# Kernel optimization log

Hardware: AMD Instinct MI355X
Metric: run time of the kernel (lower is better)

## Reference

```python
import jax, jax.numpy as jnp
import numpy as np

B, N, DIM = 2, 4096, 512
HEADS, DIM_HEAD = 8, 64
INNER = HEADS * DIM_HEAD  # 512
SCALE = DIM_HEAD ** -0.5
LN_EPS = 1e-5


def setup_inputs() -> dict:
    key = jax.random.key(0)
    ks = jax.random.split(key, 4)
    x = jax.random.normal(ks[0], (B, N, DIM), dtype=jnp.float32)
    # weights stored as [in, out] for plain matmul
    w_qkv = jax.random.normal(ks[1], (DIM, 3 * INNER), dtype=jnp.float32) * (DIM ** -0.5)
    ln_gamma = jnp.ones((INNER,), dtype=jnp.float32)
    ln_beta = jnp.zeros((INNER,), dtype=jnp.float32)
    w_out = jax.random.normal(ks[2], (INNER, DIM), dtype=jnp.float32) * (INNER ** -0.5)
    b_out = jnp.zeros((DIM,), dtype=jnp.float32)
    return {"x": x, "w_qkv": w_qkv, "ln_gamma": ln_gamma, "ln_beta": ln_beta,
            "w_out": w_out, "b_out": b_out}


def _layernorm(x, gamma, beta):
    mu = jnp.mean(x, axis=-1, keepdims=True)
    var = jnp.mean(jnp.square(x - mu), axis=-1, keepdims=True)
    return (x - mu) * jax.lax.rsqrt(var + LN_EPS) * gamma + beta


def reference(x, w_qkv, ln_gamma, ln_beta, w_out, b_out):
    b, n, _ = x.shape
    qkv = x @ w_qkv                                   # [b, n, 3*inner]
    q, k, v = jnp.split(qkv, 3, axis=-1)
    def to_heads(t):
        return t.reshape(b, n, HEADS, DIM_HEAD).transpose(0, 2, 1, 3)  # [b,h,n,d]
    q, k, v = to_heads(q), to_heads(k), to_heads(v)
    dots = jnp.einsum('bhid,bhjd->bhij', q, k) * SCALE  # [b,h,n,n]
    attn = jax.nn.relu(dots)                            # non-softmax rectified attention
    out = jnp.einsum('bhij,bhjd->bhid', attn, v)        # [b,h,n,d]
    out = out.transpose(0, 2, 1, 3).reshape(b, n, INNER)
    out = _layernorm(out, ln_gamma, ln_beta)
    return out @ w_out + b_out                          # [b,n,dim]
```

## Files before the change

### kernel.cpp

```cpp
#include <hip/hip_runtime.h>
#include <stdint.h>
#include <stddef.h>

typedef __bf16 bf16;
typedef bf16 bf16x4 __attribute__((ext_vector_type(4)));
typedef bf16 bf16x8 __attribute__((ext_vector_type(8)));
typedef float f32x4 __attribute__((ext_vector_type(4)));

#define DEVI static __device__ __forceinline__


DEVI f32x4 mfma16(bf16x8 a, bf16x8 b, f32x4 c) {
  return __builtin_amdgcn_mfma_f32_16x16x32_bf16(a, b, c, 0, 0, 0);
}

DEVI void gload_lds16(const bf16* g, bf16* lds) {
  __builtin_amdgcn_global_load_lds(
      (const __attribute__((address_space(1))) unsigned int*)g,
      (__attribute__((address_space(3))) unsigned int*)lds, 16, 0, 0);
}

DEVI int sigma64(int r) { return (r & 0x23) | ((r & 0xC) << 1) | ((r & 0x10) >> 2); }


__global__ __launch_bounds__(256) void cvt_kernel(const float* __restrict__ in,
                                                  bf16* __restrict__ out, int n4) {
  int i = blockIdx.x * blockDim.x + threadIdx.x;
  const int stride = gridDim.x * blockDim.x;
  for (; i < n4; i += stride) {
    f32x4 v = reinterpret_cast<const f32x4*>(in)[i];
    bf16x4 o;
    o[0] = (bf16)v[0]; o[1] = (bf16)v[1]; o[2] = (bf16)v[2]; o[3] = (bf16)v[3];
    reinterpret_cast<bf16x4*>(out)[i] = o;
  }
}

__global__ __launch_bounds__(256) void tcvt_kernel(const float* __restrict__ in,
                                                   bf16* __restrict__ out, int Kd, int Nd) {
  __shared__ bf16 T[64 * 80];
  const int k0 = blockIdx.y * 64, n0 = blockIdx.x * 64;
  const int r = threadIdx.x >> 2;
  const int c0 = (threadIdx.x & 3) * 16;
  const float* src = in + (size_t)(k0 + r) * Nd + n0 + c0;
#pragma unroll
  for (int j = 0; j < 16; ++j) T[(c0 + j) * 80 + r] = (bf16)src[j];
  __syncthreads();
  bf16* dst = out + (size_t)(n0 + r) * Kd + k0 + c0;
  const bf16* s = T + r * 80 + c0;
#pragma unroll
  for (int j = 0; j < 2; ++j)
    *reinterpret_cast<bf16x8*>(dst + j * 8) =
        *reinterpret_cast<const bf16x8*>(s + j * 8);
}

template <int EPI>
__global__ __launch_bounds__(256) void gemm_kernel(
    const bf16* __restrict__ A, const bf16* __restrict__ BT,
    bf16* __restrict__ qo, bf16* __restrict__ ko, bf16* __restrict__ vto,
    const float* __restrict__ bias, float* __restrict__ fo) {
  constexpr int K = 512;
  __shared__ __align__(16) bf16 SM[4 * 128 * 64];
  const int lane = threadIdx.x & 63;
  const int w = threadIdx.x >> 6;
  const int hi = lane >> 4;
  const int wm = w >> 1, wn = w & 1;
  const int m0 = blockIdx.y * 128, n0 = blockIdx.x * 128;
  const int sl = lane >> 3;
  const int ssc = ((lane & 7) ^ sl) * 8;

  auto AsB = [&](int bi) { return SM + bi * 8192; };
  auto BsB = [&](int bi) { return SM + 16384 + bi * 8192; };

  auto stage = [&](int bi, int kt) {
    const int k0 = kt * 64;
#pragma unroll
    for (int c = 0; c < 4; ++c) {
      const int ca = w * 4 + c;
      const int trow = ca * 8 + sl;
      gload_lds16(A + (size_t)(m0 + trow) * K + k0 + ssc, AsB(bi) + ca * 512);
      gload_lds16(BT + (size_t)(n0 + trow) * K + k0 + ssc, BsB(bi) + ca * 512);
    }
  };

  f32x4 acc[4][4];
#pragma unroll
  for (int i = 0; i < 4; ++i)
#pragma unroll
    for (int j = 0; j < 4; ++j) acc[i][j] = {0.f, 0.f, 0.f, 0.f};

  stage(0, 0);
  asm volatile("s_waitcnt vmcnt(0)" ::: "memory");
  __builtin_amdgcn_s_barrier();

  for (int kt = 0; kt < K / 64; ++kt) {
    const int cur = kt & 1;
    if (kt < K / 64 - 1) stage(cur ^ 1, kt + 1);
    const bf16* As = AsB(cur);
    const bf16* Bs = BsB(cur);
#pragma unroll
    for (int kc = 0; kc < 2; ++kc) {
      const int cs = kc * 4 + hi;
      const int csw = (cs ^ (lane & 7)) * 8;
      bf16x8 af[4], bfr[4];
#pragma unroll
      for (int mi = 0; mi < 4; ++mi)
        af[mi] = *reinterpret_cast<const bf16x8*>(
            &As[(wm * 64 + mi * 16 + (lane & 15)) * 64 + csw]);
#pragma unroll
      for (int ni = 0; ni < 4; ++ni)
        bfr[ni] = *reinterpret_cast<const bf16x8*>(
            &Bs[(wn * 64 + ni * 16 + (lane & 15)) * 64 + csw]);
      __builtin_amdgcn_s_setprio(1);
#pragma unroll
      for (int mi = 0; mi < 4; ++mi)
#pragma unroll
        for (int ni = 0; ni < 4; ++ni)
          acc[mi][ni] = mfma16(af[mi], bfr[ni], acc[mi][ni]);
      __builtin_amdgcn_s_setprio(0);
    }
    asm volatile("s_waitcnt vmcnt(0)" ::: "memory");
    __builtin_amdgcn_s_barrier();
  }

  if (EPI == 0) {
    if (n0 < 1024) {
#pragma unroll
      for (int mi = 0; mi < 4; ++mi)
#pragma unroll
        for (int ni = 0; ni < 4; ++ni)
#pragma unroll
          for (int r = 0; r < 4; ++r) {
            const int rl = wm * 64 + mi * 16 + hi * 4 + r;
            const int cl = wn * 64 + ni * 16 + (lane & 15);
            SM[rl * 136 + cl] = (bf16)acc[mi][ni][r];
          }
      __syncthreads();
      const int rl = threadIdx.x >> 1, hh = threadIdx.x & 1;
      const int m = m0 + rl, b = m >> 12, n = m & 4095;
      const int colg = n0 + hh * 64;
      const int sec = colg >> 9, h = (colg & 511) >> 6;
      bf16* dst = (sec ? ko : qo) + ((size_t)(b * 8 + h) * 4096 + n) * 64;
      const bf16* srcp = SM + rl * 136 + hh * 64;
#pragma unroll
      for (int j = 0; j < 8; ++j)
        *reinterpret_cast<bf16x8*>(dst + j * 8) =
            *reinterpret_cast<const bf16x8*>(srcp + j * 8);
    } else {
#pragma unroll
      for (int mi = 0; mi < 4; ++mi)
#pragma unroll
        for (int ni = 0; ni < 4; ++ni)
#pragma unroll
          for (int r = 0; r < 4; ++r) {
            const int rl = wm * 64 + mi * 16 + hi * 4 + r;
            const int cl = wn * 64 + ni * 16 + (lane & 15);
            SM[cl * 136 + rl] = (bf16)acc[mi][ni][r];
          }
      __syncthreads();
      const int b = m0 >> 12, nb = m0 & 4095;
      const int cl = threadIdx.x >> 1, half = threadIdx.x & 1;
      const int jj = (n0 - 1024) + cl, h = jj >> 6, d = jj & 63;
      bf16* dst = vto + ((size_t)(b * 8 + h) * 64 + d) * 4096 + nb + half * 64;
      const bf16* srcp = SM + cl * 136 + half * 64;
#pragma unroll
      for (int j = 0; j < 8; ++j)
        *reinterpret_cast<bf16x8*>(dst + j * 8) =
            *reinterpret_cast<const bf16x8*>(srcp + j * 8);
    }
    return;
  }

#pragma unroll
  for (int mi = 0; mi < 4; ++mi) {
#pragma unroll
    for (int ni = 0; ni < 4; ++ni) {
#pragma unroll
      for (int r = 0; r < 4; ++r) {
        const int m = m0 + wm * 64 + mi * 16 + hi * 4 + r;
        const int col = n0 + wn * 64 + ni * 16 + (lane & 15);
        fo[(size_t)m * 512 + col] = acc[mi][ni][r] + bias[col];
      }
    }
  }
}

__global__ __launch_bounds__(256, 4) void attn_kernel(
    const bf16* __restrict__ Q, const bf16* __restrict__ Kg,
    const bf16* __restrict__ VT, float* __restrict__ out0,
    float* __restrict__ out1) {
  __shared__ __align__(16) bf16 Ks[2 * 64 * 64];
  __shared__ __align__(16) bf16 Vs[2 * 64 * 64];
  const int lane = threadIdx.x & 63;
  const int w = threadIdx.x >> 6;
  const int hi = lane >> 4;
  const int ql = lane & 15;
  const int bh = blockIdx.y;
  const int q0 = blockIdx.x * 128 + w * 32;
  const int kvbase = blockIdx.z * 2048;
  const bf16* Qh = Q + (size_t)bh * 4096 * 64;
  const bf16* Kh = Kg + (size_t)bh * 4096 * 64;
  const bf16* Vh = VT + (size_t)bh * 64 * 4096;
  float* outp = blockIdx.z ? out1 : out0;

  const int sl = lane >> 3;
  const int ssc = ((lane & 7) ^ sl) * 8;

  int soff[4];
  if (w < 2) {
#pragma unroll
    for (int c = 0; c < 4; ++c) {
      const int rho = (w * 4 + c) * 8 + sl;
      soff[c] = sigma64(rho) * 64 + ssc;
    }
  } else {
#pragma unroll
    for (int c = 0; c < 4; ++c) {
      const int d = ((w - 2) * 4 + c) * 8 + sl;
      soff[c] = d * 4096 + ssc;
    }
  }

  auto stage = [&](int bi, int kv0) {
    if (w < 2) {
      bf16* KsB = Ks + bi * 4096;
#pragma unroll
      for (int c = 0; c < 4; ++c)
        gload_lds16(Kh + (size_t)kv0 * 64 + soff[c], KsB + (w * 4 + c) * 512);
    } else {
      bf16* VsB = Vs + bi * 4096;
#pragma unroll
      for (int c = 0; c < 4; ++c)
        gload_lds16(Vh + kv0 + soff[c], VsB + ((w - 2) * 4 + c) * 512);
    }
  };

  bf16x8 qf[2][2];
#pragma unroll
  for (int qb = 0; qb < 2; ++qb)
#pragma unroll
    for (int kc = 0; kc < 2; ++kc)
      qf[qb][kc] = *reinterpret_cast<const bf16x8*>(
          &Qh[(size_t)(q0 + qb * 16 + ql) * 64 + kc * 32 + hi * 8]);

  f32x4 o[2][4];
#pragma unroll
  for (int qb = 0; qb < 2; ++qb)
#pragma unroll
    for (int db = 0; db < 4; ++db) o[qb][db] = {0.f, 0.f, 0.f, 0.f};

  stage(0, kvbase);
  asm volatile("s_waitcnt vmcnt(0)" ::: "memory");
  __builtin_amdgcn_s_barrier();

  for (int it = 0; it < 32; ++it) {
    const int kv0 = kvbase + it * 64;
    const int cur = it & 1;
    const bf16* KsC = Ks + cur * 4096;
    const bf16* VsC = Vs + cur * 4096;
    if (it < 31) stage(cur ^ 1, kv0 + 64);

    f32x4 s[2][4];
#pragma unroll
    for (int qb = 0; qb < 2; ++qb)
#pragma unroll
      for (int kvb = 0; kvb < 4; ++kvb) s[qb][kvb] = {0.f, 0.f, 0.f, 0.f};
#pragma unroll
    for (int kc = 0; kc < 2; ++kc) {
      const int csw = ((kc * 4 + hi) ^ (lane & 7)) * 8;
      bf16x8 kf[4];
#pragma unroll
      for (int kvb = 0; kvb < 4; ++kvb)
        kf[kvb] = *reinterpret_cast<const bf16x8*>(
            &KsC[(kvb * 16 + ql) * 64 + csw]);
      __builtin_amdgcn_s_setprio(1);
#pragma unroll
      for (int qb = 0; qb < 2; ++qb)
#pragma unroll
        for (int kvb = 0; kvb < 4; ++kvb)
          s[qb][kvb] = mfma16(kf[kvb], qf[qb][kc], s[qb][kvb]);
      __builtin_amdgcn_s_setprio(0);
    }

#pragma unroll
    for (int kc = 0; kc < 2; ++kc) {
      const int csw = ((kc * 4 + hi) ^ (lane & 7)) * 8;
      bf16x8 vf[4];
#pragma unroll
      for (int db = 0; db < 4; ++db)
        vf[db] = *reinterpret_cast<const bf16x8*>(
            &VsC[(db * 16 + ql) * 64 + csw]);
      bf16x8 pa[2];
#pragma unroll
      for (int qb = 0; qb < 2; ++qb)
#pragma unroll
        for (int u = 0; u < 2; ++u)
#pragma unroll
          for (int r = 0; r < 4; ++r)
            pa[qb][u * 4 + r] = (bf16)fmaxf(s[qb][2 * kc + u][r], 0.f);
      __builtin_amdgcn_s_setprio(1);
#pragma unroll
      for (int qb = 0; qb < 2; ++qb)
#pragma unroll
        for (int db = 0; db < 4; ++db)
          o[qb][db] = mfma16(pa[qb], vf[db], o[qb][db]);
      __builtin_amdgcn_s_setprio(0);
    }

    asm volatile("s_waitcnt vmcnt(0)" ::: "memory");
    __builtin_amdgcn_s_barrier();
  }

  const int b = bh >> 3, h = bh & 7;
#pragma unroll
  for (int qb = 0; qb < 2; ++qb)
#pragma unroll
    for (int db = 0; db < 4; ++db)
#pragma unroll
      for (int r = 0; r < 4; ++r) {
        const int n = q0 + qb * 16 + hi * 4 + r;
        const int dcol = db * 16 + ql;
        outp[((size_t)(b * 4096 + n)) * 512 + h * 64 + dcol] = o[qb][db][r] * 0.125f;
      }
}

__global__ __launch_bounds__(256) void ln_kernel(const float* __restrict__ in0,
                                                 const float* __restrict__ in1,
                                                 const float* __restrict__ gamma,
                                                 const float* __restrict__ beta,
                                                 bf16* __restrict__ out) {
  const int lane = threadIdx.x & 63;
  const int w = threadIdx.x >> 6;
  const int row = blockIdx.x * 4 + w;
  const float* r0 = in0 + (size_t)row * 512;
  const float* r1 = in1 + (size_t)row * 512;
  f32x4 a = *reinterpret_cast<const f32x4*>(&r0[lane * 4]);
  f32x4 b = *reinterpret_cast<const f32x4*>(&r0[256 + lane * 4]);
  f32x4 a1 = *reinterpret_cast<const f32x4*>(&r1[lane * 4]);
  f32x4 b1 = *reinterpret_cast<const f32x4*>(&r1[256 + lane * 4]);
#pragma unroll
  for (int i = 0; i < 4; ++i) { a[i] += a1[i]; b[i] += b1[i]; }
  float s = a[0] + a[1] + a[2] + a[3] + b[0] + b[1] + b[2] + b[3];
  float ss = a[0] * a[0] + a[1] * a[1] + a[2] * a[2] + a[3] * a[3] +
             b[0] * b[0] + b[1] * b[1] + b[2] * b[2] + b[3] * b[3];
#pragma unroll
  for (int off = 32; off > 0; off >>= 1) {
    s += __shfl_xor(s, off);
    ss += __shfl_xor(ss, off);
  }
  const float mean = s * (1.f / 512.f);
  const float var = ss * (1.f / 512.f) - mean * mean;
  const float rstd = rsqrtf(var + 1e-5f);
  f32x4 g0 = *reinterpret_cast<const f32x4*>(&gamma[lane * 4]);
  f32x4 g1 = *reinterpret_cast<const f32x4*>(&gamma[256 + lane * 4]);
  f32x4 e0 = *reinterpret_cast<const f32x4*>(&beta[lane * 4]);
  f32x4 e1 = *reinterpret_cast<const f32x4*>(&beta[256 + lane * 4]);
  bf16x4 o0, o1;
#pragma unroll
  for (int i = 0; i < 4; ++i) {
    o0[i] = (bf16)((a[i] - mean) * rstd * g0[i] + e0[i]);
    o1[i] = (bf16)((b[i] - mean) * rstd * g1[i] + e1[i]);
  }
  *reinterpret_cast<bf16x4*>(&out[(size_t)row * 512 + lane * 4]) = o0;
  *reinterpret_cast<bf16x4*>(&out[(size_t)row * 512 + 256 + lane * 4]) = o1;
}

extern "C" void kernel_launch(void* const* d_in, const int* in_sizes, int n_in,
                              void* d_out, int out_size, void* d_ws, size_t ws_size,
                              hipStream_t stream) {
  const float* x = (const float*)d_in[0];
  const float* w_qkv = (const float*)d_in[1];
  const float* ln_g = (const float*)d_in[2];
  const float* ln_b = (const float*)d_in[3];
  const float* w_out = (const float*)d_in[4];
  const float* b_out = (const float*)d_in[5];
  float* out = (float*)d_out;

  char* ws = (char*)d_ws;
  size_t off = 0;
  auto alloc = [&](size_t bytes) {
    void* p = ws + off;
    off += (bytes + 255) & ~(size_t)255;
    return p;
  };
  bf16* x_bf = (bf16*)alloc((size_t)8192 * 512 * 2);
  bf16* wqkvT = (bf16*)alloc((size_t)1536 * 512 * 2);
  bf16* woutT = (bf16*)alloc((size_t)512 * 512 * 2);
  bf16* qbuf = (bf16*)alloc((size_t)16 * 4096 * 64 * 2);
  bf16* kbuf = (bf16*)alloc((size_t)16 * 4096 * 64 * 2);
  bf16* vtbuf = (bf16*)alloc((size_t)16 * 64 * 4096 * 2);
  float* attn_out0 = (float*)alloc((size_t)8192 * 512 * 4);
  float* attn_out1 = (float*)alloc((size_t)8192 * 512 * 4);
  bf16* ln_bf = (bf16*)alloc((size_t)8192 * 512 * 2);

  cvt_kernel<<<2048, 256, 0, stream>>>(x, x_bf, 8192 * 512 / 4);
  tcvt_kernel<<<dim3(24, 8), 256, 0, stream>>>(w_qkv, wqkvT, 512, 1536);
  tcvt_kernel<<<dim3(8, 8), 256, 0, stream>>>(w_out, woutT, 512, 512);

  gemm_kernel<0><<<dim3(12, 64), 256, 0, stream>>>(x_bf, wqkvT, qbuf, kbuf, vtbuf,
                                                   nullptr, nullptr);

  attn_kernel<<<dim3(32, 16, 2), 256, 0, stream>>>(qbuf, kbuf, vtbuf,
                                                   attn_out0, attn_out1);

  ln_kernel<<<2048, 256, 0, stream>>>(attn_out0, attn_out1, ln_g, ln_b, ln_bf);

  gemm_kernel<1><<<dim3(4, 64), 256, 0, stream>>>(ln_bf, woutT, nullptr, nullptr,
                                                  nullptr, b_out, out);
}
```

Before: 182.5 us.

## Merge prep kernels, drop attention KV split, fuse layernorm into output GEMM

```diff
diff --git a/kernel.cpp b/kernel.cpp
--- a/kernel.cpp
+++ b/kernel.cpp
@@ -23,22 +23,9 @@
 DEVI int sigma64(int r) { return (r & 0x23) | ((r & 0xC) << 1) | ((r & 0x10) >> 2); }
 
 
-__global__ __launch_bounds__(256) void cvt_kernel(const float* __restrict__ in,
-                                                  bf16* __restrict__ out, int n4) {
-  int i = blockIdx.x * blockDim.x + threadIdx.x;
-  const int stride = gridDim.x * blockDim.x;
-  for (; i < n4; i += stride) {
-    f32x4 v = reinterpret_cast<const f32x4*>(in)[i];
-    bf16x4 o;
-    o[0] = (bf16)v[0]; o[1] = (bf16)v[1]; o[2] = (bf16)v[2]; o[3] = (bf16)v[3];
-    reinterpret_cast<bf16x4*>(out)[i] = o;
-  }
-}
-
-__global__ __launch_bounds__(256) void tcvt_kernel(const float* __restrict__ in,
-                                                   bf16* __restrict__ out, int Kd, int Nd) {
-  __shared__ bf16 T[64 * 80];
-  const int k0 = blockIdx.y * 64, n0 = blockIdx.x * 64;
+DEVI void tcvt_tile(const float* __restrict__ in, bf16* __restrict__ out,
+                    int Kd, int Nd, int bx, int by, bf16* T) {
+  const int k0 = by * 64, n0 = bx * 64;
   const int r = threadIdx.x >> 2;
   const int c0 = (threadIdx.x & 3) * 16;
   const float* src = in + (size_t)(k0 + r) * Nd + n0 + c0;
@@ -53,11 +40,33 @@
         *reinterpret_cast<const bf16x8*>(s + j * 8);
 }
 
-template <int EPI>
+__global__ __launch_bounds__(256) void prep_kernel(
+    const float* __restrict__ x, bf16* __restrict__ xb,
+    const float* __restrict__ wq, bf16* __restrict__ wqT,
+    const float* __restrict__ wo, bf16* __restrict__ woT) {
+  __shared__ bf16 T[64 * 80];
+  const int blk = blockIdx.x;
+  if (blk < 2048) {
+    int i = blk * 256 + threadIdx.x;
+    const int n4 = 8192 * 512 / 4, stride = 2048 * 256;
+    for (; i < n4; i += stride) {
+      f32x4 v = reinterpret_cast<const f32x4*>(x)[i];
+      bf16x4 o;
+      o[0] = (bf16)v[0]; o[1] = (bf16)v[1]; o[2] = (bf16)v[2]; o[3] = (bf16)v[3];
+      reinterpret_cast<bf16x4*>(xb)[i] = o;
+    }
+  } else if (blk < 2240) {
+    const int t = blk - 2048;
+    tcvt_tile(wq, wqT, 512, 1536, t % 24, t / 24, T);
+  } else {
+    const int t = blk - 2240;
+    tcvt_tile(wo, woT, 512, 512, t % 8, t / 8, T);
+  }
+}
+
 __global__ __launch_bounds__(256) void gemm_kernel(
     const bf16* __restrict__ A, const bf16* __restrict__ BT,
-    bf16* __restrict__ qo, bf16* __restrict__ ko, bf16* __restrict__ vto,
-    const float* __restrict__ bias, float* __restrict__ fo) {
+    bf16* __restrict__ qo, bf16* __restrict__ ko, bf16* __restrict__ vto) {
   constexpr int K = 512;
   __shared__ __align__(16) bf16 SM[4 * 128 * 64];
   const int lane = threadIdx.x & 63;
@@ -99,8 +108,7 @@
     const bf16* Bs = BsB(cur);
 #pragma unroll
     for (int kc = 0; kc < 2; ++kc) {
-      const int cs = kc * 4 + hi;
-      const int csw = (cs ^ (lane & 7)) * 8;
+      const int csw = ((kc * 4 + hi) ^ (lane & 7)) * 8;
       bf16x8 af[4], bfr[4];
 #pragma unroll
       for (int mi = 0; mi < 4; ++mi)
@@ -122,117 +130,101 @@
     __builtin_amdgcn_s_barrier();
   }
 
-  if (EPI == 0) {
-    if (n0 < 1024) {
-#pragma unroll
-      for (int mi = 0; mi < 4; ++mi)
-#pragma unroll
-        for (int ni = 0; ni < 4; ++ni)
-#pragma unroll
-          for (int r = 0; r < 4; ++r) {
-            const int rl = wm * 64 + mi * 16 + hi * 4 + r;
-            const int cl = wn * 64 + ni * 16 + (lane & 15);
-            SM[rl * 136 + cl] = (bf16)acc[mi][ni][r];
-          }
-      __syncthreads();
-      const int rl = threadIdx.x >> 1, hh = threadIdx.x & 1;
-      const int m = m0 + rl, b = m >> 12, n = m & 4095;
-      const int colg = n0 + hh * 64;
-      const int sec = colg >> 9, h = (colg & 511) >> 6;
-      bf16* dst = (sec ? ko : qo) + ((size_t)(b * 8 + h) * 4096 + n) * 64;
-      const bf16* srcp = SM + rl * 136 + hh * 64;
-#pragma unroll
-      for (int j = 0; j < 8; ++j)
-        *reinterpret_cast<bf16x8*>(dst + j * 8) =
-            *reinterpret_cast<const bf16x8*>(srcp + j * 8);
-    } else {
-#pragma unroll
-      for (int mi = 0; mi < 4; ++mi)
-#pragma unroll
-        for (int ni = 0; ni < 4; ++ni)
-#pragma unroll
-          for (int r = 0; r < 4; ++r) {
-            const int rl = wm * 64 + mi * 16 + hi * 4 + r;
-            const int cl = wn * 64 + ni * 16 + (lane & 15);
-            SM[cl * 136 + rl] = (bf16)acc[mi][ni][r];
-          }
-      __syncthreads();
-      const int b = m0 >> 12, nb = m0 & 4095;
-      const int cl = threadIdx.x >> 1, half = threadIdx.x & 1;
-      const int jj = (n0 - 1024) + cl, h = jj >> 6, d = jj & 63;
-      bf16* dst = vto + ((size_t)(b * 8 + h) * 64 + d) * 4096 + nb + half * 64;
-      const bf16* srcp = SM + cl * 136 + half * 64;
-#pragma unroll
-      for (int j = 0; j < 8; ++j)
-        *reinterpret_cast<bf16x8*>(dst + j * 8) =
-            *reinterpret_cast<const bf16x8*>(srcp + j * 8);
-    }
-    return;
-  }
-
-#pragma unroll
-  for (int mi = 0; mi < 4; ++mi) {
-#pragma unroll
-    for (int ni = 0; ni < 4; ++ni) {
-#pragma unroll
-      for (int r = 0; r < 4; ++r) {
-        const int m = m0 + wm * 64 + mi * 16 + hi * 4 + r;
-        const int col = n0 + wn * 64 + ni * 16 + (lane & 15);
-        fo[(size_t)m * 512 + col] = acc[mi][ni][r] + bias[col];
-      }
-    }
-  }
-}
-
-__global__ __launch_bounds__(256, 4) void attn_kernel(
+  if (n0 < 1024) {
+#pragma unroll
+    for (int mi = 0; mi < 4; ++mi)
+#pragma unroll
+      for (int ni = 0; ni < 4; ++ni)
+#pragma unroll
+        for (int r = 0; r < 4; ++r) {
+          const int rl = wm * 64 + mi * 16 + hi * 4 + r;
+          const int cl = wn * 64 + ni * 16 + (lane & 15);
+          SM[rl * 136 + cl] = (bf16)acc[mi][ni][r];
+        }
+    __syncthreads();
+    const int rl = threadIdx.x >> 1, hh = threadIdx.x & 1;
+    const int m = m0 + rl, b = m >> 12, n = m & 4095;
+    const int colg = n0 + hh * 64;
+    const int sec = colg >> 9, h = (colg & 511) >> 6;
+    bf16* dst = (sec ? ko : qo) + ((size_t)(b * 8 + h) * 4096 + n) * 64;
+    const bf16* srcp = SM + rl * 136 + hh * 64;
+#pragma unroll
+    for (int j = 0; j < 8; ++j)
+      *reinterpret_cast<bf16x8*>(dst + j * 8) =
+          *reinterpret_cast<const bf16x8*>(srcp + j * 8);
+  } else {
+#pragma unroll
+    for (int mi = 0; mi < 4; ++mi)
+#pragma unroll
+      for (int ni = 0; ni < 4; ++ni)
+#pragma unroll
+        for (int r = 0; r < 4; ++r) {
+          const int rl = wm * 64 + mi * 16 + hi * 4 + r;
+          const int cl = wn * 64 + ni * 16 + (lane & 15);
+          SM[cl * 136 + rl] = (bf16)acc[mi][ni][r];
+        }
+    __syncthreads();
+    const int b = m0 >> 12, nb = m0 & 4095;
+    const int cl = threadIdx.x >> 1, half = threadIdx.x & 1;
+    const int jj = (n0 - 1024) + cl, h = jj >> 6, d = jj & 63;
+    bf16* dst = vto + ((size_t)(b * 8 + h) * 64 + d) * 4096 + nb + half * 64;
+    const bf16* srcp = SM + cl * 136 + half * 64;
+#pragma unroll
+    for (int j = 0; j < 8; ++j)
+      *reinterpret_cast<bf16x8*>(dst + j * 8) =
+          *reinterpret_cast<const bf16x8*>(srcp + j * 8);
+  }
+}
+
+__global__ __launch_bounds__(256, 2) void attn_kernel(
     const bf16* __restrict__ Q, const bf16* __restrict__ Kg,
-    const bf16* __restrict__ VT, float* __restrict__ out0,
-    float* __restrict__ out1) {
-  __shared__ __align__(16) bf16 Ks[2 * 64 * 64];
-  __shared__ __align__(16) bf16 Vs[2 * 64 * 64];
+    const bf16* __restrict__ VT, float* __restrict__ out) {
+  __shared__ __align__(16) bf16 KV[6 * 4096];
   const int lane = threadIdx.x & 63;
   const int w = threadIdx.x >> 6;
   const int hi = lane >> 4;
   const int ql = lane & 15;
   const int bh = blockIdx.y;
   const int q0 = blockIdx.x * 128 + w * 32;
-  const int kvbase = blockIdx.z * 2048;
   const bf16* Qh = Q + (size_t)bh * 4096 * 64;
   const bf16* Kh = Kg + (size_t)bh * 4096 * 64;
   const bf16* Vh = VT + (size_t)bh * 64 * 4096;
-  float* outp = blockIdx.z ? out1 : out0;
 
   const int sl = lane >> 3;
   const int ssc = ((lane & 7) ^ sl) * 8;
 
-  int soff[4];
+  const bf16* gs[4];
+  int dstoff[4], step;
   if (w < 2) {
 #pragma unroll
     for (int c = 0; c < 4; ++c) {
       const int rho = (w * 4 + c) * 8 + sl;
-      soff[c] = sigma64(rho) * 64 + ssc;
-    }
+      gs[c] = Kh + sigma64(rho) * 64 + ssc;
+      dstoff[c] = (w * 4 + c) * 512;
+    }
+    step = 64 * 64;
   } else {
 #pragma unroll
     for (int c = 0; c < 4; ++c) {
       const int d = ((w - 2) * 4 + c) * 8 + sl;
-      soff[c] = d * 4096 + ssc;
-    }
-  }
-
-  auto stage = [&](int bi, int kv0) {
-    if (w < 2) {
-      bf16* KsB = Ks + bi * 4096;
-#pragma unroll
-      for (int c = 0; c < 4; ++c)
-        gload_lds16(Kh + (size_t)kv0 * 64 + soff[c], KsB + (w * 4 + c) * 512);
-    } else {
-      bf16* VsB = Vs + bi * 4096;
-#pragma unroll
-      for (int c = 0; c < 4; ++c)
-        gload_lds16(Vh + kv0 + soff[c], VsB + ((w - 2) * 4 + c) * 512);
+      gs[c] = Vh + (size_t)d * 4096 + ssc;
+      dstoff[c] = 12288 + ((w - 2) * 4 + c) * 512;
+    }
+    step = 64;
+  }
+
+  auto stageN = [&](int bi) {
+#pragma unroll
+    for (int c = 0; c < 4; ++c) {
+      gload_lds16(gs[c], KV + bi * 4096 + dstoff[c]);
+      gs[c] += step;
     }
   };
+
+  int lro[2];
+#pragma unroll
+  for (int kc = 0; kc < 2; ++kc)
+    lro[kc] = ql * 64 + (((kc * 4 + hi) ^ (lane & 7)) * 8);
 
   bf16x8 qf[2][2];
 #pragma unroll
@@ -248,16 +240,19 @@
 #pragma unroll
     for (int db = 0; db < 4; ++db) o[qb][db] = {0.f, 0.f, 0.f, 0.f};
 
-  stage(0, kvbase);
-  asm volatile("s_waitcnt vmcnt(0)" ::: "memory");
-  __builtin_amdgcn_s_barrier();
-
-  for (int it = 0; it < 32; ++it) {
-    const int kv0 = kvbase + it * 64;
-    const int cur = it & 1;
-    const bf16* KsC = Ks + cur * 4096;
-    const bf16* VsC = Vs + cur * 4096;
-    if (it < 31) stage(cur ^ 1, kv0 + 64);
+  stageN(0);
+  int buf = 0, bufn = 1;
+
+  for (int it = 0; it < 64; ++it) {
+    if (it < 63) {
+      stageN(bufn);
+      asm volatile("s_waitcnt vmcnt(4)" ::: "memory");
+    } else {
+      asm volatile("s_waitcnt vmcnt(0)" ::: "memory");
+    }
+    __builtin_amdgcn_s_barrier();
+
+    const bf16* Kb = KV + buf * 4096;
 
     f32x4 s[2][4];
 #pragma unroll
@@ -266,12 +261,11 @@
       for (int kvb = 0; kvb < 4; ++kvb) s[qb][kvb] = {0.f, 0.f, 0.f, 0.f};
 #pragma unroll
     for (int kc = 0; kc < 2; ++kc) {
-      const int csw = ((kc * 4 + hi) ^ (lane & 7)) * 8;
+      const bf16* kbp = Kb + lro[kc];
       bf16x8 kf[4];
 #pragma unroll
       for (int kvb = 0; kvb < 4; ++kvb)
-        kf[kvb] = *reinterpret_cast<const bf16x8*>(
-            &KsC[(kvb * 16 + ql) * 64 + csw]);
+        kf[kvb] = *reinterpret_cast<const bf16x8*>(kbp + kvb * 1024);
       __builtin_amdgcn_s_setprio(1);
 #pragma unroll
       for (int qb = 0; qb < 2; ++qb)
@@ -283,12 +277,11 @@
 
 #pragma unroll
     for (int kc = 0; kc < 2; ++kc) {
-      const int csw = ((kc * 4 + hi) ^ (lane & 7)) * 8;
+      const bf16* vbp = Kb + 12288 + lro[kc];
       bf16x8 vf[4];
 #pragma unroll
       for (int db = 0; db < 4; ++db)
-        vf[db] = *reinterpret_cast<const bf16x8*>(
-            &VsC[(db * 16 + ql) * 64 + csw]);
+        vf[db] = *reinterpret_cast<const bf16x8*>(vbp + db * 1024);
       bf16x8 pa[2];
 #pragma unroll
       for (int qb = 0; qb < 2; ++qb)
@@ -306,8 +299,8 @@
       __builtin_amdgcn_s_setprio(0);
     }
 
-    asm volatile("s_waitcnt vmcnt(0)" ::: "memory");
-    __builtin_amdgcn_s_barrier();
+    buf = bufn;
+    bufn = (bufn == 2) ? 0 : bufn + 1;
   }
 
   const int b = bh >> 3, h = bh & 7;
@@ -319,49 +312,122 @@
       for (int r = 0; r < 4; ++r) {
         const int n = q0 + qb * 16 + hi * 4 + r;
         const int dcol = db * 16 + ql;
-        outp[((size_t)(b * 4096 + n)) * 512 + h * 64 + dcol] = o[qb][db][r] * 0.125f;
+        out[((size_t)(b * 4096 + n)) * 512 + h * 64 + dcol] = o[qb][db][r] * 0.125f;
       }
 }
 
-__global__ __launch_bounds__(256) void ln_kernel(const float* __restrict__ in0,
-                                                 const float* __restrict__ in1,
-                                                 const float* __restrict__ gamma,
-                                                 const float* __restrict__ beta,
-                                                 bf16* __restrict__ out) {
-  const int lane = threadIdx.x & 63;
-  const int w = threadIdx.x >> 6;
-  const int row = blockIdx.x * 4 + w;
-  const float* r0 = in0 + (size_t)row * 512;
-  const float* r1 = in1 + (size_t)row * 512;
-  f32x4 a = *reinterpret_cast<const f32x4*>(&r0[lane * 4]);
-  f32x4 b = *reinterpret_cast<const f32x4*>(&r0[256 + lane * 4]);
-  f32x4 a1 = *reinterpret_cast<const f32x4*>(&r1[lane * 4]);
-  f32x4 b1 = *reinterpret_cast<const f32x4*>(&r1[256 + lane * 4]);
-#pragma unroll
-  for (int i = 0; i < 4; ++i) { a[i] += a1[i]; b[i] += b1[i]; }
-  float s = a[0] + a[1] + a[2] + a[3] + b[0] + b[1] + b[2] + b[3];
-  float ss = a[0] * a[0] + a[1] * a[1] + a[2] * a[2] + a[3] * a[3] +
-             b[0] * b[0] + b[1] * b[1] + b[2] * b[2] + b[3] * b[3];
-#pragma unroll
-  for (int off = 32; off > 0; off >>= 1) {
-    s += __shfl_xor(s, off);
-    ss += __shfl_xor(ss, off);
-  }
-  const float mean = s * (1.f / 512.f);
-  const float var = ss * (1.f / 512.f) - mean * mean;
-  const float rstd = rsqrtf(var + 1e-5f);
-  f32x4 g0 = *reinterpret_cast<const f32x4*>(&gamma[lane * 4]);
-  f32x4 g1 = *reinterpret_cast<const f32x4*>(&gamma[256 + lane * 4]);
-  f32x4 e0 = *reinterpret_cast<const f32x4*>(&beta[lane * 4]);
-  f32x4 e1 = *reinterpret_cast<const f32x4*>(&beta[256 + lane * 4]);
-  bf16x4 o0, o1;
-#pragma unroll
-  for (int i = 0; i < 4; ++i) {
-    o0[i] = (bf16)((a[i] - mean) * rstd * g0[i] + e0[i]);
-    o1[i] = (bf16)((b[i] - mean) * rstd * g1[i] + e1[i]);
-  }
-  *reinterpret_cast<bf16x4*>(&out[(size_t)row * 512 + lane * 4]) = o0;
-  *reinterpret_cast<bf16x4*>(&out[(size_t)row * 512 + 256 + lane * 4]) = o1;
+__global__ __launch_bounds__(256) void lngemm_kernel(
+    const float* __restrict__ X,
+    const bf16* __restrict__ BT,
+    const float* __restrict__ gamma, const float* __restrict__ beta,
+    const float* __restrict__ bias, float* __restrict__ out) {
+  __shared__ __align__(16) bf16 As[128 * 64];
+  __shared__ __align__(16) bf16 Bs[128 * 64];
+  __shared__ float gG[512];
+  __shared__ float gB[512];
+  __shared__ float MR[128 * 2];
+  const int tid = threadIdx.x;
+  const int lane = tid & 63;
+  const int w = tid >> 6;
+  const int hi = lane >> 4;
+  const int wm = w >> 1, wn = w & 1;
+  const int m0 = blockIdx.y * 128, n0 = blockIdx.x * 128;
+  const int sl = lane >> 3;
+  const int ssc = ((lane & 7) ^ sl) * 8;
+
+  {
+    const int i = tid * 2;
+    gG[i] = gamma[i]; gG[i + 1] = gamma[i + 1];
+    gB[i] = beta[i];  gB[i + 1] = beta[i + 1];
+  }
+
+  {
+    const int row = tid >> 1, hf = tid & 1;
+    const float* src = X + (size_t)(m0 + row) * 512 + hf * 256;
+    float s = 0.f, ss = 0.f;
+#pragma unroll
+    for (int j = 0; j < 64; ++j) {
+      f32x4 v = reinterpret_cast<const f32x4*>(src)[j];
+#pragma unroll
+      for (int q = 0; q < 4; ++q) { s += v[q]; ss += v[q] * v[q]; }
+    }
+    s += __shfl_xor(s, 1);
+    ss += __shfl_xor(ss, 1);
+    if (hf == 0) {
+      const float mean = s * (1.f / 512.f);
+      const float var = ss * (1.f / 512.f) - mean * mean;
+      MR[row * 2] = mean;
+      MR[row * 2 + 1] = rsqrtf(var + 1e-5f);
+    }
+  }
+
+  f32x4 acc[4][4];
+#pragma unroll
+  for (int i = 0; i < 4; ++i)
+#pragma unroll
+    for (int j = 0; j < 4; ++j) acc[i][j] = {0.f, 0.f, 0.f, 0.f};
+
+  for (int kt = 0; kt < 8; ++kt) {
+    __syncthreads();
+#pragma unroll
+    for (int c = 0; c < 4; ++c) {
+      const int ca = w * 4 + c;
+      const int trow = ca * 8 + sl;
+      gload_lds16(BT + (size_t)(n0 + trow) * 512 + kt * 64 + ssc, Bs + ca * 512);
+    }
+    {
+      const int row = tid >> 1, hf = tid & 1;
+      const float mean = MR[row * 2], rstd = MR[row * 2 + 1];
+      const float* src = X + (size_t)(m0 + row) * 512 + kt * 64 + hf * 32;
+      const float* gg = gG + kt * 64 + hf * 32;
+      const float* bb = gB + kt * 64 + hf * 32;
+#pragma unroll
+      for (int q = 0; q < 4; ++q) {
+        const int si = hf * 4 + q;
+        f32x4 v0 = reinterpret_cast<const f32x4*>(src)[q * 2];
+        f32x4 v1 = reinterpret_cast<const f32x4*>(src)[q * 2 + 1];
+        bf16x8 ov;
+#pragma unroll
+        for (int j = 0; j < 4; ++j) {
+          ov[j] = (bf16)((v0[j] - mean) * rstd * gg[q * 8 + j] + bb[q * 8 + j]);
+          ov[4 + j] = (bf16)((v1[j] - mean) * rstd * gg[q * 8 + 4 + j] + bb[q * 8 + 4 + j]);
+        }
+        *reinterpret_cast<bf16x8*>(&As[row * 64 + ((si ^ (row & 7)) * 8)]) = ov;
+      }
+    }
+    __syncthreads();
+#pragma unroll
+    for (int kc = 0; kc < 2; ++kc) {
+      const int csw = ((kc * 4 + hi) ^ (lane & 7)) * 8;
+      bf16x8 af[4], bfr[4];
+#pragma unroll
+      for (int mi = 0; mi < 4; ++mi)
+        af[mi] = *reinterpret_cast<const bf16x8*>(
+            &As[(wm * 64 + mi * 16 + (lane & 15)) * 64 + csw]);
+#pragma unroll
+      for (int ni = 0; ni < 4; ++ni)
+        bfr[ni] = *reinterpret_cast<const bf16x8*>(
+            &Bs[(wn * 64 + ni * 16 + (lane & 15)) * 64 + csw]);
+      __builtin_amdgcn_s_setprio(1);
+#pragma unroll
+      for (int mi = 0; mi < 4; ++mi)
+#pragma unroll
+        for (int ni = 0; ni < 4; ++ni)
+          acc[mi][ni] = mfma16(af[mi], bfr[ni], acc[mi][ni]);
+      __builtin_amdgcn_s_setprio(0);
+    }
+  }
+
+#pragma unroll
+  for (int mi = 0; mi < 4; ++mi)
+#pragma unroll
+    for (int ni = 0; ni < 4; ++ni)
+#pragma unroll
+      for (int r = 0; r < 4; ++r) {
+        const int m = m0 + wm * 64 + mi * 16 + hi * 4 + r;
+        const int col = n0 + wn * 64 + ni * 16 + (lane & 15);
+        out[(size_t)m * 512 + col] = acc[mi][ni][r] + bias[col];
+      }
 }
 
 extern "C" void kernel_launch(void* const* d_in, const int* in_sizes, int n_in,
@@ -388,22 +454,14 @@
   bf16* qbuf = (bf16*)alloc((size_t)16 * 4096 * 64 * 2);
   bf16* kbuf = (bf16*)alloc((size_t)16 * 4096 * 64 * 2);
   bf16* vtbuf = (bf16*)alloc((size_t)16 * 64 * 4096 * 2);
-  float* attn_out0 = (float*)alloc((size_t)8192 * 512 * 4);
-  float* attn_out1 = (float*)alloc((size_t)8192 * 512 * 4);
-  bf16* ln_bf = (bf16*)alloc((size_t)8192 * 512 * 2);
-
-  cvt_kernel<<<2048, 256, 0, stream>>>(x, x_bf, 8192 * 512 / 4);
-  tcvt_kernel<<<dim3(24, 8), 256, 0, stream>>>(w_qkv, wqkvT, 512, 1536);
-  tcvt_kernel<<<dim3(8, 8), 256, 0, stream>>>(w_out, woutT, 512, 512);
-
-  gemm_kernel<0><<<dim3(12, 64), 256, 0, stream>>>(x_bf, wqkvT, qbuf, kbuf, vtbuf,
-                                                   nullptr, nullptr);
-
-  attn_kernel<<<dim3(32, 16, 2), 256, 0, stream>>>(qbuf, kbuf, vtbuf,
-                                                   attn_out0, attn_out1);
-
-  ln_kernel<<<2048, 256, 0, stream>>>(attn_out0, attn_out1, ln_g, ln_b, ln_bf);
-
-  gemm_kernel<1><<<dim3(4, 64), 256, 0, stream>>>(ln_bf, woutT, nullptr, nullptr,
-                                                  nullptr, b_out, out);
-}
+  float* attn_out = (float*)alloc((size_t)8192 * 512 * 4);
+
+  prep_kernel<<<2304, 256, 0, stream>>>(x, x_bf, w_qkv, wqkvT, w_out, woutT);
+
+  gemm_kernel<<<dim3(12, 64), 256, 0, stream>>>(x_bf, wqkvT, qbuf, kbuf, vtbuf);
+
+  attn_kernel<<<dim3(32, 16), 256, 0, stream>>>(qbuf, kbuf, vtbuf, attn_out);
+
+  lngemm_kernel<<<dim3(4, 64), 256, 0, stream>>>(attn_out, woutT, ln_g, ln_b,
+                                                 b_out, out);
+}
```

Result: slower. 206.1 us (+12.9%).
